# Optimization experiments

Hardware: AMD Instinct MI355X
Metric: run time of the kernel (lower is better)

Reference implementation:

```python
import jax, jax.numpy as jnp
import numpy as np

B, NPG, H, D = 8, 6250, 4, 128   # graphs, nodes/graph, heads, hidden
N = B * NPG                       # 50000 nodes total
E = 400000                        # edges
VOCAB = 10000


def setup_inputs() -> dict:
    key = jax.random.key(0)
    ks = jax.random.split(key, 12)
    p = lambda k, shape: jax.random.normal(k, shape, dtype=jnp.float32) * 0.05
    return {
        "node_ids": jax.random.randint(ks[0], (N,), 0, VOCAB),
        "src": jax.random.randint(ks[1], (E,), 0, N),
        "dst": jax.random.randint(ks[2], (E,), 0, N),
        "emb": p(ks[3], (VOCAB, D)),
        "W_src": p(ks[4], (D, H * D)), "b_src": jnp.zeros((H * D,), jnp.float32),
        "W_dst": p(ks[5], (D, H * D)), "b_dst": jnp.zeros((H * D,), jnp.float32),
        "attn": p(ks[6], (H, D)),
        "W_res": p(ks[7], (D, H * D)), "b_res": jnp.zeros((H * D,), jnp.float32),
        "W_gc": p(ks[8], (D, D)), "b_gc": jnp.zeros((D,), jnp.float32),
        "W_mlp": p(ks[9], (3 * D, 1)), "b_mlp": jnp.zeros((1,), jnp.float32),
    }


def _leaky(x, s):
    return jnp.where(x >= 0, x, s * x)


def _maxpool(feat):
    # dgl.max_nodes: per-graph max over nodes -> [B, feat_dim]
    return jnp.max(feat.reshape(B, NPG, -1), axis=1)


def _gatv2(x, src, dst, W_src, b_src, W_dst, b_dst, attn, W_res, b_res):
    # DGL GATv2Conv (share_weights=False, residual=True, eval mode -> no dropout)
    hs = (x @ W_src + b_src).reshape(N, H, D)
    hd = (x @ W_dst + b_dst).reshape(N, H, D)
    e = _leaky(hs[src] + hd[dst], 0.2)              # [E,H,D]
    logits = jnp.einsum('ehd,hd->eh', e, attn)      # [E,H]
    m = jax.ops.segment_max(logits, dst, num_segments=N)
    ex = jnp.exp(logits - m[dst])
    denom = jax.ops.segment_sum(ex, dst, num_segments=N)
    alpha = ex / denom[dst]                          # edge softmax per dst/head
    rst = jax.ops.segment_sum(hs[src] * alpha[..., None], dst, num_segments=N)
    rst = rst + (x @ W_res + b_res).reshape(N, H, D)
    return _leaky(rst, 0.01)                         # nn.LeakyReLU() activation


def _graphconv(x, src, dst, W, b):
    # DGL GraphConv norm='both', allow_zero_in_degree=True, LeakyReLU activation
    ones = jnp.ones((E,), x.dtype)
    dout = jnp.clip(jax.ops.segment_sum(ones, src, num_segments=N), 1.0, None)
    din = jnp.clip(jax.ops.segment_sum(ones, dst, num_segments=N), 1.0, None)
    h = x * jax.lax.rsqrt(dout)[:, None]
    agg = jax.ops.segment_sum(h[src], dst, num_segments=N)
    h = agg * jax.lax.rsqrt(din)[:, None]
    return _leaky(h @ W + b, 0.01)


def reference(node_ids, src, dst, emb, W_src, b_src, W_dst, b_dst, attn,
              W_res, b_res, W_gc, b_gc, W_mlp, b_mlp):
    feat = emb[node_ids]                             # featurize_nodes
    pools = [_maxpool(feat)]
    res = _gatv2(feat, src, dst, W_src, b_src, W_dst, b_dst, attn,
                 W_res, b_res).mean(axis=1)          # mean over heads -> [N,D]
    pools.append(_maxpool(res))
    res = _graphconv(res, src, dst, W_gc, b_gc)
    pools.append(_maxpool(res))
    agg = jnp.concatenate(pools, axis=1)             # [B, 3D]
    # reward_predictor_block_two: ReLU -> (Dropout eval) -> Linear(3D, 1)
    return jax.nn.relu(agg) @ W_mlp + b_mlp          # BCE logits [B,1]
```

## Files before the change

kernel.cpp:

```cpp
#include <hip/hip_runtime.h>
#include <float.h>
#include <math.h>

#define Bg   8
#define NPGc 6250
#define Hh   4
#define Dd   128
#define Nn   50000
#define Ee   400000
#define HDd  512
#define WNf  1536
#define NCHUNK 49

typedef unsigned short ushort_t;
typedef __attribute__((ext_vector_type(8))) short bf16x8;
typedef __attribute__((ext_vector_type(4))) float f32x4;

__device__ __forceinline__ void atomicMaxF(float* addr, float val) {
    if (val >= 0.0f) atomicMax((int*)addr, __float_as_int(val));
    else             atomicMin((unsigned int*)addr, __float_as_uint(val));
}

__device__ __forceinline__ ushort_t f2bf(float x) {
    unsigned u = __float_as_uint(x);
    unsigned r = (u + 0x7FFFu + ((u >> 16) & 1u)) >> 16;
    return (ushort_t)r;
}

__device__ __forceinline__ void bf2x2(unsigned u, float& lo, float& hi) {
    lo = __uint_as_float(u << 16);
    hi = __uint_as_float(u & 0xFFFF0000u);
}

__global__ void setup_kernel(const int* __restrict__ ids, const float* __restrict__ emb,
                             float* __restrict__ feat, ushort_t* __restrict__ feat_bf,
                             const float* __restrict__ W_src, const float* __restrict__ W_dst,
                             const float* __restrict__ W_res, const float* __restrict__ W_gc,
                             const float* __restrict__ b_src, const float* __restrict__ b_dst,
                             const float* __restrict__ b_res,
                             ushort_t* __restrict__ Wt, ushort_t* __restrict__ Wt_gc,
                             float* __restrict__ bias_f,
                             int* __restrict__ din_i, float* __restrict__ dout,
                             int* __restrict__ cursor, float* __restrict__ pools) {
    int i = blockIdx.x * blockDim.x + threadIdx.x;
    {
        int n = i >> 5, c = i & 31;
        int id = ids[n];
        float4 v = ((const float4*)emb)[(size_t)id * 32 + c];
        ((float4*)feat)[(size_t)n * 32 + c] = v;
        ushort4 b;
        b.x = f2bf(v.x); b.y = f2bf(v.y); b.z = f2bf(v.z); b.w = f2bf(v.w);
        ((ushort4*)feat_bf)[(size_t)n * 32 + c] = b;
    }
    if (i < Nn) { din_i[i] = 0; dout[i] = 0.0f; cursor[i] = 0; }
    if (i < Bg * 3 * Dd) pools[i] = -FLT_MAX;
    if (i < WNf * 128) {
        int c = i >> 7, k = i & 127;
        float v = (c < 512) ? W_src[k * 512 + c]
                : (c < 1024) ? W_dst[k * 512 + (c - 512)]
                             : W_res[k * 512 + (c - 1024)];
        Wt[i] = f2bf(v);
    } else if (i < WNf * 128 + 128 * 128) {
        int j = i - WNf * 128;
        int c = j >> 7, k = j & 127;
        Wt_gc[j] = f2bf(W_gc[k * 128 + c]);
    }
    if (i < WNf)
        bias_f[i] = (i < 512) ? b_src[i] : (i < 1024) ? b_dst[i - 512] : b_res[i - 1024];
}

__global__ void maxpool_kernel(const float* __restrict__ x, float* __restrict__ pools, int col_off) {
    int b = blockIdx.x, chunk = blockIdx.y, d = threadIdx.x;
    int i0 = chunk * 125, i1 = i0 + 125;
    float mx = -FLT_MAX;
    for (int i = i0; i < i1; ++i)
        mx = fmaxf(mx, x[((size_t)(b * NPGc + i)) * Dd + d]);
    atomicMaxF(&pools[b * (3 * Dd) + col_off + d], mx);
}

template<int NTILE, bool LEAK, bool BF16OUT>
__global__ __launch_bounds__(256, 3) void mfma_gemm_kernel(
    const ushort_t* __restrict__ A, const ushort_t* __restrict__ Wt,
    const float* __restrict__ bias, ushort_t* __restrict__ Ob, float* __restrict__ Of,
    int n_rows, int WN)
{
    int ct0   = blockIdx.y * NTILE;
    int row0  = blockIdx.x * 64;
    int w = threadIdx.x >> 6, lane = threadIdx.x & 63;
    int lrow = lane & 15, kg = lane >> 4;

    bf16x8 av[4][4];
    {
        const ushort_t* ap = A + (size_t)(row0 + lrow) * 128 + kg * 8;
        #pragma unroll
        for (int fi = 0; fi < 4; ++fi)
            #pragma unroll
            for (int ks = 0; ks < 4; ++ks)
                av[fi][ks] = *(const bf16x8*)(ap + fi * 16 * 128 + ks * 32);
    }

    const ushort_t* wp = Wt + (size_t)(ct0 * 64 + w * 16 + lrow) * 128 + kg * 8;
    const size_t TSTR = 64 * 128;

    #pragma unroll
    for (int ct = 0; ct < NTILE; ++ct) {
        bf16x8 wv[4];
        #pragma unroll
        for (int ks = 0; ks < 4; ++ks)
            wv[ks] = *(const bf16x8*)(wp + (size_t)ct * TSTR + ks * 32);

        f32x4 acc[4] = {};
        #pragma unroll
        for (int ks = 0; ks < 4; ++ks)
            #pragma unroll
            for (int fi = 0; fi < 4; ++fi)
                acc[fi] = __builtin_amdgcn_mfma_f32_16x16x32_bf16(wv[ks], av[fi][ks], acc[fi], 0, 0, 0);

        int colb = (ct0 + ct) * 64 + w * 16 + kg * 4;
        float4 bv4 = *(const float4*)(bias + colb);
        #pragma unroll
        for (int fi = 0; fi < 4; ++fi) {
            int grow = row0 + fi * 16 + lrow;
            if (grow < n_rows) {
                float o[4];
                #pragma unroll
                for (int j = 0; j < 4; ++j) {
                    float v = acc[fi][j] + ((const float*)&bv4)[j];
                    if (LEAK) v = v >= 0.0f ? v : 0.01f * v;
                    o[j] = v;
                }
                if (BF16OUT) {
                    unsigned r0, r1;
                    asm("v_cvt_pk_bf16_f32 %0, %1, %2" : "=v"(r0) : "v"(o[0]), "v"(o[1]));
                    asm("v_cvt_pk_bf16_f32 %0, %1, %2" : "=v"(r1) : "v"(o[2]), "v"(o[3]));
                    uint2 ob; ob.x = r0; ob.y = r1;
                    *(uint2*)(Ob + (size_t)grow * WN + colb) = ob;
                } else {
                    *(float4*)(Of + (size_t)grow * WN + colb) = *(float4*)o;
                }
            }
        }
    }
}

__global__ void degree2_kernel(const int* __restrict__ src, const int* __restrict__ dst,
                               int* __restrict__ din_i, float* __restrict__ dout) {
    int e = blockIdx.x * blockDim.x + threadIdx.x;
    if (e >= Ee) return;
    atomicAdd(&din_i[dst[e]], 1);
    atomicAdd(&dout[src[e]], 1.0f);
}

__global__ __launch_bounds__(256) void scan_reduce_kernel(const int* __restrict__ din_i,
                                                          int* __restrict__ partials) {
    int b = blockIdx.x, t = threadIdx.x;
    int base = b * 1024 + t * 4;
    int s = 0;
    #pragma unroll
    for (int j = 0; j < 4; ++j) { int i = base + j; if (i < Nn) s += din_i[i]; }
    #pragma unroll
    for (int off = 32; off > 0; off >>= 1) s += __shfl_xor(s, off);
    __shared__ int wsum[4];
    if ((t & 63) == 0) wsum[t >> 6] = s;
    __syncthreads();
    if (t == 0) partials[b] = wsum[0] + wsum[1] + wsum[2] + wsum[3];
}

__global__ void scan_mid_kernel(int* __restrict__ partials, int* __restrict__ row_start) {
    if (threadIdx.x == 0) {
        int acc = 0;
        for (int i = 0; i < NCHUNK; ++i) { int v = partials[i]; partials[i] = acc; acc += v; }
        row_start[Nn] = acc;
    }
}

__global__ __launch_bounds__(256) void scan_final_kernel(const int* __restrict__ din_i,
                                                         const int* __restrict__ partials,
                                                         int* __restrict__ row_start,
                                                         float* __restrict__ din_f) {
    int b = blockIdx.x, t = threadIdx.x;
    int base = b * 1024 + t * 4;
    int v[4]; int s = 0;
    #pragma unroll
    for (int j = 0; j < 4; ++j) {
        v[j] = (base + j < Nn) ? din_i[base + j] : 0;
        s += v[j];
    }
    __shared__ int buf[256];
    buf[t] = s;
    __syncthreads();
    #pragma unroll
    for (int off = 1; off < 256; off <<= 1) {
        int x = (t >= off) ? buf[t - off] : 0;
        __syncthreads();
        buf[t] += x;
        __syncthreads();
    }
    int excl = buf[t] - s + partials[b];
    #pragma unroll
    for (int j = 0; j < 4; ++j) {
        if (base + j < Nn) {
            row_start[base + j] = excl;
            din_f[base + j] = (float)v[j];
            excl += v[j];
        }
    }
}

__global__ void scatter_kernel(const int* __restrict__ src, const int* __restrict__ dst,
                               const int* __restrict__ row_start, int* __restrict__ cursor,
                               int* __restrict__ csr_src) {
    int e = blockIdx.x * blockDim.x + threadIdx.x;
    if (e >= Ee) return;
    int d = dst[e];
    int slot = row_start[d] + atomicAdd(&cursor[d], 1);
    csr_src[slot] = src[e];
}

__global__ __launch_bounds__(256) void gat_fused_kernel(
    const ushort_t* __restrict__ h_all, const float* __restrict__ attn,
    const int* __restrict__ row_start, const int* __restrict__ csr_src,
    float* __restrict__ res)
{
    int d = (blockIdx.x * 256 + threadIdx.x) >> 6;
    int lane = threadIdx.x & 63;
    if (d >= Nn) return;
    int e0 = row_start[d], e1 = row_start[d + 1];

    float hdv[8], atv[8];
    {
        uint4 hr = *(const uint4*)(h_all + (size_t)d * WNf + 512 + lane * 8);
        bf2x2(hr.x, hdv[0], hdv[1]); bf2x2(hr.y, hdv[2], hdv[3]);
        bf2x2(hr.z, hdv[4], hdv[5]); bf2x2(hr.w, hdv[6], hdv[7]);
        float4 a0 = *(const float4*)(attn + lane * 8);
        float4 a1 = *(const float4*)(attn + lane * 8 + 4);
        atv[0] = a0.x; atv[1] = a0.y; atv[2] = a0.z; atv[3] = a0.w;
        atv[4] = a1.x; atv[5] = a1.y; atv[6] = a1.z; atv[7] = a1.w;
    }

    float m = -FLT_MAX, denom = 0.0f;
    float acc[8] = {};

    int s = (e0 < e1) ? csr_src[e0] : 0;
    uint4 raw = *(const uint4*)(h_all + (size_t)s * WNf + lane * 8);
    for (int e = e0; e < e1; ++e) {
        int s_next = (e + 1 < e1) ? csr_src[e + 1] : s;
        uint4 raw_next = *(const uint4*)(h_all + (size_t)s_next * WNf + lane * 8);
        float hsv[8];
        bf2x2(raw.x, hsv[0], hsv[1]); bf2x2(raw.y, hsv[2], hsv[3]);
        bf2x2(raw.z, hsv[4], hsv[5]); bf2x2(raw.w, hsv[6], hsv[7]);
        float p = 0.0f;
        #pragma unroll
        for (int j = 0; j < 8; ++j) {
            float x = hsv[j] + hdv[j];
            x = x >= 0.0f ? x : 0.2f * x;
            p = fmaf(x, atv[j], p);
        }
        p += __shfl_xor(p, 1); p += __shfl_xor(p, 2);
        p += __shfl_xor(p, 4); p += __shfl_xor(p, 8);
        float mn = fmaxf(m, p);
        float corr = expf(m - mn);
        float ex = expf(p - mn);
        denom = denom * corr + ex;
        #pragma unroll
        for (int j = 0; j < 8; ++j) acc[j] = fmaf(acc[j], corr, hsv[j] * ex);
        m = mn;
        raw = raw_next;
    }

    float inv = (e1 > e0) ? 1.0f / denom : 0.0f;
    float rv[8];
    {
        uint4 rr = *(const uint4*)(h_all + (size_t)d * WNf + 1024 + lane * 8);
        bf2x2(rr.x, rv[0], rv[1]); bf2x2(rr.y, rv[2], rv[3]);
        bf2x2(rr.z, rv[4], rv[5]); bf2x2(rr.w, rv[6], rv[7]);
    }
    float t[8];
    #pragma unroll
    for (int j = 0; j < 8; ++j) {
        float v = fmaf(acc[j], inv, rv[j]);
        t[j] = v >= 0.0f ? v : 0.01f * v;
    }
    #pragma unroll
    for (int j = 0; j < 8; ++j) {
        t[j] += __shfl_xor(t[j], 16);
        t[j] += __shfl_xor(t[j], 32);
    }
    if (lane < 16) {
        float o0[4] = {0.25f * t[0], 0.25f * t[1], 0.25f * t[2], 0.25f * t[3]};
        float o1[4] = {0.25f * t[4], 0.25f * t[5], 0.25f * t[6], 0.25f * t[7]};
        *(float4*)(res + (size_t)d * Dd + lane * 8)     = *(float4*)o0;
        *(float4*)(res + (size_t)d * Dd + lane * 8 + 4) = *(float4*)o1;
    }
}

__global__ __launch_bounds__(256) void gc_gather_kernel(
    const float* __restrict__ res, const int* __restrict__ row_start,
    const int* __restrict__ csr_src, const float* __restrict__ dout,
    const float* __restrict__ din, ushort_t* __restrict__ agg_bf)
{
    int d = (blockIdx.x * 256 + threadIdx.x) >> 6;
    int lane = threadIdx.x & 63;
    if (d >= Nn) return;
    int e0 = row_start[d], e1 = row_start[d + 1];
    float ax = 0.0f, ay = 0.0f;
    int s = (e0 < e1) ? csr_src[e0] : 0;
    float sc = 1.0f / sqrtf(fmaxf((e0 < e1) ? dout[s] : 1.0f, 1.0f));
    float2 v = (e0 < e1) ? ((const float2*)(res + (size_t)s * Dd))[lane] : make_float2(0.f, 0.f);
    for (int e = e0; e < e1; ++e) {
        int s_next = (e + 1 < e1) ? csr_src[e + 1] : s;
        float sc_n = 1.0f / sqrtf(fmaxf(dout[s_next], 1.0f));
        float2 v_n = ((const float2*)(res + (size_t)s_next * Dd))[lane];
        ax = fmaf(v.x, sc, ax);
        ay = fmaf(v.y, sc, ay);
        sc = sc_n;
        v = v_n;
    }
    float scd = 1.0f / sqrtf(fmaxf(din[d], 1.0f));
    ushort2 o;
    o.x = f2bf(ax * scd);
    o.y = f2bf(ay * scd);
    ((ushort2*)(agg_bf + (size_t)d * Dd))[lane] = o;
}

__global__ void final_kernel(const float* __restrict__ pools, const float* __restrict__ W_mlp,
                             const float* __restrict__ b_mlp, float* __restrict__ out) {
    int b = blockIdx.x, lane = threadIdx.x;
    float s = 0.0f;
    for (int j = lane; j < 3 * Dd; j += 64)
        s += fmaxf(pools[b * (3 * Dd) + j], 0.0f) * W_mlp[j];
    #pragma unroll
    for (int off = 32; off > 0; off >>= 1) s += __shfl_xor(s, off);
    if (lane == 0) out[b] = s + b_mlp[0];
}

extern "C" void kernel_launch(void* const* d_in, const int* in_sizes, int n_in,
                              void* d_out, int out_size, void* d_ws, size_t ws_size,
                              hipStream_t stream) {
    const int*   node_ids = (const int*)d_in[0];
    const int*   src      = (const int*)d_in[1];
    const int*   dst      = (const int*)d_in[2];
    const float* emb      = (const float*)d_in[3];
    const float* W_src    = (const float*)d_in[4];
    const float* b_src    = (const float*)d_in[5];
    const float* W_dst    = (const float*)d_in[6];
    const float* b_dst    = (const float*)d_in[7];
    const float* attn     = (const float*)d_in[8];
    const float* W_res    = (const float*)d_in[9];
    const float* b_res    = (const float*)d_in[10];
    const float* W_gc     = (const float*)d_in[11];
    const float* b_gc     = (const float*)d_in[12];
    const float* W_mlp    = (const float*)d_in[13];
    const float* b_mlp    = (const float*)d_in[14];
    float* out = (float*)d_out;

    char* w = (char*)d_ws;
    size_t off = 0;
    float*    feat    = (float*)(w + off);    off += (size_t)Nn * Dd * 4;
    ushort_t* feat_bf = (ushort_t*)(w + off); off += (size_t)(Nn + 64) * Dd * 2;
    ushort_t* h_all   = (ushort_t*)(w + off); off += (size_t)Nn * WNf * 2;
    ushort_t* Wt      = (ushort_t*)(w + off); off += (size_t)WNf * 128 * 2;
    ushort_t* Wt_gc   = (ushort_t*)(w + off); off += (size_t)128 * 128 * 2;
    float*    bias_f  = (float*)(w + off);    off += (size_t)WNf * 4;
    int*      csr_src = (int*)(w + off);      off += (size_t)Ee * 4;
    int*      row_st  = (int*)(w + off);      off += ((size_t)Nn + 4) * 4;
    int*      cursor  = (int*)(w + off);      off += (size_t)Nn * 4;
    int*      din_i   = (int*)(w + off);      off += (size_t)Nn * 4;
    float*    din_f   = (float*)(w + off);    off += (size_t)Nn * 4;
    float*    dout_f  = (float*)(w + off);    off += (size_t)Nn * 4;
    int*      partials= (int*)(w + off);      off += 64 * 4;
    float*    pools   = (float*)(w + off);    off += (size_t)Bg * 3 * Dd * 4;

    float*    res    = feat;
    ushort_t* agg_bf = h_all;
    float*    res2   = (float*)(w + (size_t)Nn * Dd * 6 + (size_t)(Nn + 64) * Dd * 2);

    setup_kernel<<<(Nn * 32) / 256, 256, 0, stream>>>(
        node_ids, emb, feat, feat_bf, W_src, W_dst, W_res, W_gc,
        b_src, b_dst, b_res, Wt, Wt_gc, bias_f, din_i, dout_f, cursor, pools);
    maxpool_kernel<<<dim3(Bg, 50), Dd, 0, stream>>>(feat, pools, 0);

    degree2_kernel<<<(Ee + 255) / 256, 256, 0, stream>>>(src, dst, din_i, dout_f);
    scan_reduce_kernel<<<NCHUNK, 256, 0, stream>>>(din_i, partials);
    scan_mid_kernel<<<1, 64, 0, stream>>>(partials, row_st);
    scan_final_kernel<<<NCHUNK, 256, 0, stream>>>(din_i, partials, row_st, din_f);
    scatter_kernel<<<(Ee + 255) / 256, 256, 0, stream>>>(src, dst, row_st, cursor, csr_src);

    mfma_gemm_kernel<12, false, true><<<dim3((Nn + 63) / 64, 2), 256, 0, stream>>>(
        feat_bf, Wt, bias_f, h_all, nullptr, Nn, WNf);

    gat_fused_kernel<<<(Nn * 64) / 256, 256, 0, stream>>>(h_all, attn, row_st, csr_src, res);
    maxpool_kernel<<<dim3(Bg, 50), Dd, 0, stream>>>(res, pools, Dd);

    gc_gather_kernel<<<(Nn * 64) / 256, 256, 0, stream>>>(res, row_st, csr_src, dout_f, din_f, agg_bf);
    mfma_gemm_kernel<2, true, false><<<dim3((Nn + 63) / 64, 1), 256, 0, stream>>>(
        agg_bf, Wt_gc, b_gc, nullptr, res2, Nn, Dd);
    maxpool_kernel<<<dim3(Bg, 50), Dd, 0, stream>>>(res2, pools, 2 * Dd);

    final_kernel<<<Bg, 64, 0, stream>>>(pools, W_mlp, b_mlp, out);
}
```

Measured before the change: 388.7 us.

## Fuse GraphConv GEMM with max-pool, deepen gather prefetch, retile main GEMM

The GraphConv GEMM now reduces its LeakyReLU output straight into per-graph column maxima with shuffles and atomics. This removes the fp32 res2 write and the separate maxpool pass. The GAT and GraphConv gather loops prefetch two edges ahead instead of one, to hide more gather latency. The main projection GEMM uses 6 column tiles per block over 4 y-blocks, with W fragments loaded ahead in three rotating buffers, and drops the launch-bounds occupancy hint. Deeper prefetch and extra buffers raise register pressure, and the graph-aligned row tiling needs padding rows in agg_bf for the last tile of each graph.

Result: slower. 397.7 us (+2.3%).

```diff
diff --git a/kernel.cpp b/kernel.cpp
--- a/kernel.cpp
+++ b/kernel.cpp
@@ -78,13 +78,13 @@
     atomicMaxF(&pools[b * (3 * Dd) + col_off + d], mx);
 }
 
-template<int NTILE, bool LEAK, bool BF16OUT>
-__global__ __launch_bounds__(256, 3) void mfma_gemm_kernel(
+#define GNT 6
+__global__ __launch_bounds__(256) void mfma_gemm_kernel(
     const ushort_t* __restrict__ A, const ushort_t* __restrict__ Wt,
-    const float* __restrict__ bias, ushort_t* __restrict__ Ob, float* __restrict__ Of,
+    const float* __restrict__ bias, ushort_t* __restrict__ Ob,
     int n_rows, int WN)
 {
-    int ct0   = blockIdx.y * NTILE;
+    int ct0   = blockIdx.y * GNT;
     int row0  = blockIdx.x * 64;
     int w = threadIdx.x >> 6, lane = threadIdx.x & 63;
     int lrow = lane & 15, kg = lane >> 4;
@@ -102,43 +102,104 @@
     const ushort_t* wp = Wt + (size_t)(ct0 * 64 + w * 16 + lrow) * 128 + kg * 8;
     const size_t TSTR = 64 * 128;
 
-    #pragma unroll
-    for (int ct = 0; ct < NTILE; ++ct) {
-        bf16x8 wv[4];
-        #pragma unroll
-        for (int ks = 0; ks < 4; ++ks)
-            wv[ks] = *(const bf16x8*)(wp + (size_t)ct * TSTR + ks * 32);
-
+    auto step = [&](bf16x8 (&wv)[4], int ct) {
         f32x4 acc[4] = {};
         #pragma unroll
         for (int ks = 0; ks < 4; ++ks)
             #pragma unroll
             for (int fi = 0; fi < 4; ++fi)
                 acc[fi] = __builtin_amdgcn_mfma_f32_16x16x32_bf16(wv[ks], av[fi][ks], acc[fi], 0, 0, 0);
-
         int colb = (ct0 + ct) * 64 + w * 16 + kg * 4;
         float4 bv4 = *(const float4*)(bias + colb);
         #pragma unroll
         for (int fi = 0; fi < 4; ++fi) {
             int grow = row0 + fi * 16 + lrow;
             if (grow < n_rows) {
-                float o[4];
-                #pragma unroll
-                for (int j = 0; j < 4; ++j) {
-                    float v = acc[fi][j] + ((const float*)&bv4)[j];
-                    if (LEAK) v = v >= 0.0f ? v : 0.01f * v;
-                    o[j] = v;
-                }
-                if (BF16OUT) {
-                    unsigned r0, r1;
-                    asm("v_cvt_pk_bf16_f32 %0, %1, %2" : "=v"(r0) : "v"(o[0]), "v"(o[1]));
-                    asm("v_cvt_pk_bf16_f32 %0, %1, %2" : "=v"(r1) : "v"(o[2]), "v"(o[3]));
-                    uint2 ob; ob.x = r0; ob.y = r1;
-                    *(uint2*)(Ob + (size_t)grow * WN + colb) = ob;
-                } else {
-                    *(float4*)(Of + (size_t)grow * WN + colb) = *(float4*)o;
-                }
+                float o0 = acc[fi][0] + bv4.x;
+                float o1 = acc[fi][1] + bv4.y;
+                float o2 = acc[fi][2] + bv4.z;
+                float o3 = acc[fi][3] + bv4.w;
+                unsigned r0, r1;
+                asm("v_cvt_pk_bf16_f32 %0, %1, %2" : "=v"(r0) : "v"(o0), "v"(o1));
+                asm("v_cvt_pk_bf16_f32 %0, %1, %2" : "=v"(r1) : "v"(o2), "v"(o3));
+                uint2 ob; ob.x = r0; ob.y = r1;
+                *(uint2*)(Ob + (size_t)grow * WN + colb) = ob;
             }
+        }
+    };
+
+#define LOADW(dst, ct) { _Pragma("unroll") \
+    for (int ks = 0; ks < 4; ++ks) dst[ks] = *(const bf16x8*)(wp + (size_t)(ct) * TSTR + ks * 32); }
+
+    bf16x8 wv0[4], wv1[4], wv2[4];
+    LOADW(wv0, 0); LOADW(wv1, 1); LOADW(wv2, 2);
+    step(wv0, 0); LOADW(wv0, 3);
+    step(wv1, 1); LOADW(wv1, 4);
+    step(wv2, 2); LOADW(wv2, 5);
+    step(wv0, 3);
+    step(wv1, 4);
+    step(wv2, 5);
+#undef LOADW
+}
+
+__global__ __launch_bounds__(256) void mfma_gc_pool_kernel(
+    const ushort_t* __restrict__ A, const ushort_t* __restrict__ Wt,
+    const float* __restrict__ bias, float* __restrict__ pools)
+{
+    int g = blockIdx.x / 98, lb = blockIdx.x % 98;
+    int row0 = g * NPGc + lb * 64;
+    int w = threadIdx.x >> 6, lane = threadIdx.x & 63;
+    int lrow = lane & 15, kg = lane >> 4;
+
+    bf16x8 av[4][4];
+    {
+        const ushort_t* ap = A + (size_t)(row0 + lrow) * 128 + kg * 8;
+        #pragma unroll
+        for (int fi = 0; fi < 4; ++fi)
+            #pragma unroll
+            for (int ks = 0; ks < 4; ++ks)
+                av[fi][ks] = *(const bf16x8*)(ap + fi * 16 * 128 + ks * 32);
+    }
+
+    #pragma unroll
+    for (int ct = 0; ct < 2; ++ct) {
+        bf16x8 wv[4];
+        const ushort_t* wp = Wt + (size_t)(ct * 64 + w * 16 + lrow) * 128 + kg * 8;
+        #pragma unroll
+        for (int ks = 0; ks < 4; ++ks) wv[ks] = *(const bf16x8*)(wp + ks * 32);
+
+        f32x4 acc[4] = {};
+        #pragma unroll
+        for (int ks = 0; ks < 4; ++ks)
+            #pragma unroll
+            for (int fi = 0; fi < 4; ++fi)
+                acc[fi] = __builtin_amdgcn_mfma_f32_16x16x32_bf16(wv[ks], av[fi][ks], acc[fi], 0, 0, 0);
+
+        int colb = ct * 64 + w * 16 + kg * 4;
+        float4 bv4 = *(const float4*)(bias + colb);
+        float mcol[4] = {-FLT_MAX, -FLT_MAX, -FLT_MAX, -FLT_MAX};
+        #pragma unroll
+        for (int fi = 0; fi < 4; ++fi) {
+            int lr = lb * 64 + fi * 16 + lrow;
+            bool valid = lr < NPGc;
+            #pragma unroll
+            for (int j = 0; j < 4; ++j) {
+                float v = acc[fi][j] + ((const float*)&bv4)[j];
+                v = v >= 0.0f ? v : 0.01f * v;
+                if (valid) mcol[j] = fmaxf(mcol[j], v);
+            }
+        }
+        #pragma unroll
+        for (int j = 0; j < 4; ++j) {
+            mcol[j] = fmaxf(mcol[j], __shfl_xor(mcol[j], 1));
+            mcol[j] = fmaxf(mcol[j], __shfl_xor(mcol[j], 2));
+            mcol[j] = fmaxf(mcol[j], __shfl_xor(mcol[j], 4));
+            mcol[j] = fmaxf(mcol[j], __shfl_xor(mcol[j], 8));
+        }
+        if (lrow == 0) {
+            #pragma unroll
+            for (int j = 0; j < 4; ++j)
+                atomicMaxF(&pools[g * (3 * Dd) + 2 * Dd + colb + j], mcol[j]);
         }
     }
 }
@@ -241,14 +302,16 @@
     float m = -FLT_MAX, denom = 0.0f;
     float acc[8] = {};
 
-    int s = (e0 < e1) ? csr_src[e0] : 0;
-    uint4 raw = *(const uint4*)(h_all + (size_t)s * WNf + lane * 8);
+    int s0 = (e0 < e1) ? csr_src[e0] : 0;
+    int s1 = (e0 + 1 < e1) ? csr_src[e0 + 1] : s0;
+    uint4 r0 = *(const uint4*)(h_all + (size_t)s0 * WNf + lane * 8);
+    uint4 r1 = *(const uint4*)(h_all + (size_t)s1 * WNf + lane * 8);
     for (int e = e0; e < e1; ++e) {
-        int s_next = (e + 1 < e1) ? csr_src[e + 1] : s;
-        uint4 raw_next = *(const uint4*)(h_all + (size_t)s_next * WNf + lane * 8);
+        int s2 = (e + 2 < e1) ? csr_src[e + 2] : s0;
+        uint4 r2 = *(const uint4*)(h_all + (size_t)s2 * WNf + lane * 8);
         float hsv[8];
-        bf2x2(raw.x, hsv[0], hsv[1]); bf2x2(raw.y, hsv[2], hsv[3]);
-        bf2x2(raw.z, hsv[4], hsv[5]); bf2x2(raw.w, hsv[6], hsv[7]);
+        bf2x2(r0.x, hsv[0], hsv[1]); bf2x2(r0.y, hsv[2], hsv[3]);
+        bf2x2(r0.z, hsv[4], hsv[5]); bf2x2(r0.w, hsv[6], hsv[7]);
         float p = 0.0f;
         #pragma unroll
         for (int j = 0; j < 8; ++j) {
@@ -265,7 +328,7 @@
         #pragma unroll
         for (int j = 0; j < 8; ++j) acc[j] = fmaf(acc[j], corr, hsv[j] * ex);
         m = mn;
-        raw = raw_next;
+        r0 = r1; r1 = r2;
     }
 
     float inv = (e1 > e0) ? 1.0f / denom : 0.0f;
@@ -304,17 +367,19 @@
     if (d >= Nn) return;
     int e0 = row_start[d], e1 = row_start[d + 1];
     float ax = 0.0f, ay = 0.0f;
-    int s = (e0 < e1) ? csr_src[e0] : 0;
-    float sc = 1.0f / sqrtf(fmaxf((e0 < e1) ? dout[s] : 1.0f, 1.0f));
-    float2 v = (e0 < e1) ? ((const float2*)(res + (size_t)s * Dd))[lane] : make_float2(0.f, 0.f);
+    int s0 = (e0 < e1) ? csr_src[e0] : 0;
+    int s1 = (e0 + 1 < e1) ? csr_src[e0 + 1] : s0;
+    float sc0 = 1.0f / sqrtf(fmaxf((e0 < e1) ? dout[s0] : 1.0f, 1.0f));
+    float sc1 = 1.0f / sqrtf(fmaxf((e0 + 1 < e1) ? dout[s1] : 1.0f, 1.0f));
+    float2 v0 = (e0 < e1) ? ((const float2*)(res + (size_t)s0 * Dd))[lane] : make_float2(0.f, 0.f);
+    float2 v1 = (e0 + 1 < e1) ? ((const float2*)(res + (size_t)s1 * Dd))[lane] : make_float2(0.f, 0.f);
     for (int e = e0; e < e1; ++e) {
-        int s_next = (e + 1 < e1) ? csr_src[e + 1] : s;
-        float sc_n = 1.0f / sqrtf(fmaxf(dout[s_next], 1.0f));
-        float2 v_n = ((const float2*)(res + (size_t)s_next * Dd))[lane];
-        ax = fmaf(v.x, sc, ax);
-        ay = fmaf(v.y, sc, ay);
-        sc = sc_n;
-        v = v_n;
+        int s2 = (e + 2 < e1) ? csr_src[e + 2] : s0;
+        float sc2 = 1.0f / sqrtf(fmaxf(dout[s2], 1.0f));
+        float2 v2 = ((const float2*)(res + (size_t)s2 * Dd))[lane];
+        ax = fmaf(v0.x, sc0, ax);
+        ay = fmaf(v0.y, sc0, ay);
+        v0 = v1; v1 = v2; sc0 = sc1; sc1 = sc2;
     }
     float scd = 1.0f / sqrtf(fmaxf(din[d], 1.0f));
     ushort2 o;
@@ -373,7 +438,6 @@
 
     float*    res    = feat;
     ushort_t* agg_bf = h_all;
-    float*    res2   = (float*)(w + (size_t)Nn * Dd * 6 + (size_t)(Nn + 64) * Dd * 2);
 
     setup_kernel<<<(Nn * 32) / 256, 256, 0, stream>>>(
         node_ids, emb, feat, feat_bf, W_src, W_dst, W_res, W_gc,
@@ -386,16 +450,14 @@
     scan_final_kernel<<<NCHUNK, 256, 0, stream>>>(din_i, partials, row_st, din_f);
     scatter_kernel<<<(Ee + 255) / 256, 256, 0, stream>>>(src, dst, row_st, cursor, csr_src);
 
-    mfma_gemm_kernel<12, false, true><<<dim3((Nn + 63) / 64, 2), 256, 0, stream>>>(
-        feat_bf, Wt, bias_f, h_all, nullptr, Nn, WNf);
+    mfma_gemm_kernel<<<dim3((Nn + 63) / 64, 4), 256, 0, stream>>>(
+        feat_bf, Wt, bias_f, h_all, Nn, WNf);
 
     gat_fused_kernel<<<(Nn * 64) / 256, 256, 0, stream>>>(h_all, attn, row_st, csr_src, res);
     maxpool_kernel<<<dim3(Bg, 50), Dd, 0, stream>>>(res, pools, Dd);
 
     gc_gather_kernel<<<(Nn * 64) / 256, 256, 0, stream>>>(res, row_st, csr_src, dout_f, din_f, agg_bf);
-    mfma_gemm_kernel<2, true, false><<<dim3((Nn + 63) / 64, 1), 256, 0, stream>>>(
-        agg_bf, Wt_gc, b_gc, nullptr, res2, Nn, Dd);
-    maxpool_kernel<<<dim3(Bg, 50), Dd, 0, stream>>>(res2, pools, 2 * Dd);
+    mfma_gc_pool_kernel<<<Bg * 98, 256, 0, stream>>>(agg_bf, Wt_gc, b_gc, pools);
 
     final_kernel<<<Bg, 64, 0, stream>>>(pools, W_mlp, b_mlp, out);
 }
```
